# Optimization experiments

Hardware: AMD Instinct MI355X
Metric: run time of the kernel (lower is better)

## Reference

```python
import jax, jax.numpy as jnp
import numpy as np

H = 32  # hidden size per direction (hard-wired in module)


def _gru_scan(x_proj, W_hh, b_hh, reverse):
    """x_proj: [T, B, 3H] = x @ W_ih.T + b_ih (precomputed). Returns all hidden states [T, B, H].
    Gate order follows PyTorch: (r, z, n)."""
    def step(h, xp):
        gh = h @ W_hh.T + b_hh                      # [B, 3H]
        xr, xz, xn = jnp.split(xp, 3, axis=-1)
        hr, hz, hn = jnp.split(gh, 3, axis=-1)
        r = jax.nn.sigmoid(xr + hr)
        z = jax.nn.sigmoid(xz + hz)
        n = jnp.tanh(xn + r * hn)
        h_new = (1.0 - z) * n + z * h
        return h_new, h_new

    B = x_proj.shape[1]
    h0 = jnp.zeros((B, H), x_proj.dtype)
    _, ys = jax.lax.scan(step, h0, x_proj, reverse=reverse)
    return ys  # ys[t] = hidden after consuming x[t] (fwd) or x[T-1..t] (bwd)


def setup_inputs() -> dict:
    key = jax.random.key(0)
    ks = jax.random.split(key, 14)
    B, T = 2048, 512
    s_ih = 1.0 / np.sqrt(H)
    inp = {
        "x": jax.random.normal(ks[0], (B, T, 1), dtype=jnp.float32),
        # forward-direction GRU params (PyTorch layout: [3H, in], [3H, H], [3H])
        "W_ih_f": jax.random.uniform(ks[1], (3 * H, 1), jnp.float32, -s_ih, s_ih),
        "W_hh_f": jax.random.uniform(ks[2], (3 * H, H), jnp.float32, -s_ih, s_ih),
        "b_ih_f": jax.random.uniform(ks[3], (3 * H,), jnp.float32, -s_ih, s_ih),
        "b_hh_f": jax.random.uniform(ks[4], (3 * H,), jnp.float32, -s_ih, s_ih),
        # backward-direction GRU params
        "W_ih_b": jax.random.uniform(ks[5], (3 * H, 1), jnp.float32, -s_ih, s_ih),
        "W_hh_b": jax.random.uniform(ks[6], (3 * H, H), jnp.float32, -s_ih, s_ih),
        "b_ih_b": jax.random.uniform(ks[7], (3 * H,), jnp.float32, -s_ih, s_ih),
        "b_hh_b": jax.random.uniform(ks[8], (3 * H,), jnp.float32, -s_ih, s_ih),
        # MLP head: Linear(64,16) -> ReLU -> Linear(16,1) -> Sigmoid
        "W1": jax.random.uniform(ks[9], (16, 2 * H), jnp.float32, -0.125, 0.125),
        "b1": jax.random.uniform(ks[10], (16,), jnp.float32, -0.125, 0.125),
        "W2": jax.random.uniform(ks[11], (1, 16), jnp.float32, -0.25, 0.25),
        "b2": jax.random.uniform(ks[12], (1,), jnp.float32, -0.25, 0.25),
    }
    return inp


def reference(x, W_ih_f, W_hh_f, b_ih_f, b_hh_f,
              W_ih_b, W_hh_b, b_ih_b, b_hh_b,
              W1, b1, W2, b2):
    xt = jnp.swapaxes(x, 0, 1)                 # [T, B, 1]
    # Precompute input projections for all timesteps (input_size=1 so this is cheap)
    xpf = xt @ W_ih_f.T + b_ih_f               # [T, B, 3H]
    xpb = xt @ W_ih_b.T + b_ih_b               # [T, B, 3H]
    ys_f = _gru_scan(xpf, W_hh_f, b_hh_f, reverse=False)
    ys_b = _gru_scan(xpb, W_hh_b, b_hh_b, reverse=True)
    # out[:, -1, :] in torch = concat(fwd hidden at t=T-1, bwd hidden at t=T-1)
    out_last = jnp.concatenate([ys_f[-1], ys_b[-1]], axis=-1)   # [B, 64]
    h1 = jax.nn.relu(out_last @ W1.T + b1)                      # [B, 16]
    return jax.nn.sigmoid(h1 @ W2.T + b2)                       # [B, 1]
```

## Files before the change

### kernel.cpp

```cpp
#include <hip/hip_runtime.h>


typedef float vf2 __attribute__((ext_vector_type(2)));
typedef float vf4 __attribute__((ext_vector_type(4)));
typedef _Float16 f16;
typedef f16 h2 __attribute__((ext_vector_type(2)));
typedef f16 h8 __attribute__((ext_vector_type(8)));

#define TT 512
#define HH 32

#define PIN(v) asm volatile("" : "+v"(v))

#define LOG2E 1.44269504f

__device__ __forceinline__ float fast_sigm(float a) {
  return __builtin_amdgcn_rcpf(1.0f + __builtin_amdgcn_exp2f(-LOG2E * a));
}
__device__ __forceinline__ float fast_tanh(float a) {
  return __builtin_fmaf(-2.0f,
      __builtin_amdgcn_rcpf(1.0f + __builtin_amdgcn_exp2f(2.0f * LOG2E * a)),
      1.0f);
}

__device__ __forceinline__ h2 pack_h2(vf2 a, float s) {
  h2 r = {(f16)(a.x * s), (f16)(a.y * s)};
  return r;
}

#define LDW16(P, BASE, S) \
  h2 P##0=pack_h2(Wp[(BASE)+0],(S)),  P##1=pack_h2(Wp[(BASE)+1],(S)), \
     P##2=pack_h2(Wp[(BASE)+2],(S)),  P##3=pack_h2(Wp[(BASE)+3],(S)), \
     P##4=pack_h2(Wp[(BASE)+4],(S)),  P##5=pack_h2(Wp[(BASE)+5],(S)), \
     P##6=pack_h2(Wp[(BASE)+6],(S)),  P##7=pack_h2(Wp[(BASE)+7],(S)), \
     P##8=pack_h2(Wp[(BASE)+8],(S)),  P##9=pack_h2(Wp[(BASE)+9],(S)), \
     P##A=pack_h2(Wp[(BASE)+10],(S)), P##B=pack_h2(Wp[(BASE)+11],(S)), \
     P##C=pack_h2(Wp[(BASE)+12],(S)), P##D=pack_h2(Wp[(BASE)+13],(S)), \
     P##E=pack_h2(Wp[(BASE)+14],(S)), P##F=pack_h2(Wp[(BASE)+15],(S)); \
  PIN(P##0);PIN(P##1);PIN(P##2);PIN(P##3);PIN(P##4);PIN(P##5);PIN(P##6);PIN(P##7); \
  PIN(P##8);PIN(P##9);PIN(P##A);PIN(P##B);PIN(P##C);PIN(P##D);PIN(P##E);PIN(P##F)

#define FDOT16(A0, A1, P, SEED) \
  float A0 = __builtin_amdgcn_fdot2(q0, P##0, (SEED), false); \
  float A1 = __builtin_amdgcn_fdot2(q1, P##1, 0.0f, false); \
  A0 = __builtin_amdgcn_fdot2(q2, P##2, A0, false);  A1 = __builtin_amdgcn_fdot2(q3, P##3, A1, false); \
  A0 = __builtin_amdgcn_fdot2(q4, P##4, A0, false);  A1 = __builtin_amdgcn_fdot2(q5, P##5, A1, false); \
  A0 = __builtin_amdgcn_fdot2(q6, P##6, A0, false);  A1 = __builtin_amdgcn_fdot2(q7, P##7, A1, false); \
  A0 = __builtin_amdgcn_fdot2(q8, P##8, A0, false);  A1 = __builtin_amdgcn_fdot2(q9, P##9, A1, false); \
  A0 = __builtin_amdgcn_fdot2(qA, P##A, A0, false);  A1 = __builtin_amdgcn_fdot2(qB, P##B, A1, false); \
  A0 = __builtin_amdgcn_fdot2(qC, P##C, A0, false);  A1 = __builtin_amdgcn_fdot2(qD, P##D, A1, false); \
  A0 = __builtin_amdgcn_fdot2(qE, P##E, A0, false);  A1 = __builtin_amdgcn_fdot2(qF, P##F, A1, false)

__global__ __launch_bounds__(256)
__attribute__((amdgpu_waves_per_eu(1, 1)))
void gru_bidir_head(const float* __restrict__ X,
                    const float* __restrict__ Wih_f, const float* __restrict__ Whh_f,
                    const float* __restrict__ bih_f, const float* __restrict__ bhh_f,
                    const float* __restrict__ Wih_b,
                    const float* __restrict__ bih_b, const float* __restrict__ bhh_b,
                    const float* __restrict__ W1, const float* __restrict__ b1,
                    const float* __restrict__ W2, const float* __restrict__ b2,
                    float* __restrict__ out)
{
  __shared__ float xbuf[8][TT];
  __shared__ f16   hbuf[8][HH];
  __shared__ float obuf[8][64];

  const int g  = threadIdx.x & 31;
  const int rs = threadIdx.x >> 5;
  const int b  = (blockIdx.x << 3) + rs;

  const vf4* Xr4 = (const vf4*)(X + (size_t)b * TT);
  vf4* xb4 = (vf4*)&xbuf[rs][0];
  #pragma unroll
  for (int q = 0; q < 4; ++q) xb4[g + 32 * q] = Xr4[g + 32 * q];

  const vf2* Wp = (const vf2*)Whh_f;
  const float s1 = -LOG2E;
  const float s2 = 2.0f * LOG2E;
  LDW16(Wr, (g)        * 16, s1);
  LDW16(Wz, (HH + g)   * 16, s1);
  LDW16(Wn, (2*HH + g) * 16, s2);

  float xwr = Wih_f[g] * s1, xwz = Wih_f[HH + g] * s1, xwn = Wih_f[2*HH + g] * s2;
  float cbr = (bih_f[g]      + bhh_f[g])      * s1;
  float cbz = (bih_f[HH + g] + bhh_f[HH + g]) * s1;
  float cbn = bih_f[2*HH + g] * s2;
  float cbh = bhh_f[2*HH + g] * s2;
  PIN(xwr); PIN(xwz); PIN(xwn); PIN(cbr); PIN(cbz); PIN(cbn); PIN(cbh);

  float h = 0.0f;
  hbuf[rs][g] = (f16)0.0f;
  __builtin_amdgcn_wave_barrier();

  const h8*  hv = (const h8*)&hbuf[rs][0];
  const vf4* xv = (const vf4*)&xbuf[rs][0];
  vf4 x4 = xv[0];

  #pragma unroll 1
  for (int tg = 0; tg < TT / 4; ++tg) {
    const vf4 x4n = xv[tg + 1 < TT / 4 ? tg + 1 : tg];

    float sr0 = __builtin_fmaf(x4.x, xwr, cbr), sz0 = __builtin_fmaf(x4.x, xwz, cbz),
          sn0 = __builtin_fmaf(x4.x, xwn, cbn);
    float sr1 = __builtin_fmaf(x4.y, xwr, cbr), sz1 = __builtin_fmaf(x4.y, xwz, cbz),
          sn1 = __builtin_fmaf(x4.y, xwn, cbn);
    float sr2 = __builtin_fmaf(x4.z, xwr, cbr), sz2 = __builtin_fmaf(x4.z, xwz, cbz),
          sn2 = __builtin_fmaf(x4.z, xwn, cbn);
    float sr3 = __builtin_fmaf(x4.w, xwr, cbr), sz3 = __builtin_fmaf(x4.w, xwz, cbz),
          sn3 = __builtin_fmaf(x4.w, xwn, cbn);

    #pragma unroll
    for (int u = 0; u < 4; ++u) {
      const float sr = (u == 0) ? sr0 : (u == 1) ? sr1 : (u == 2) ? sr2 : sr3;
      const float sz = (u == 0) ? sz0 : (u == 1) ? sz1 : (u == 2) ? sz2 : sz3;
      const float sn = (u == 0) ? sn0 : (u == 1) ? sn1 : (u == 2) ? sn2 : sn3;

      const h8 H0 = hv[0], H1 = hv[1], H2 = hv[2], H3 = hv[3];
      const h2 q0 = {H0[0], H0[1]}, q1 = {H0[2], H0[3]}, q2 = {H0[4], H0[5]}, q3 = {H0[6], H0[7]},
               q4 = {H1[0], H1[1]}, q5 = {H1[2], H1[3]}, q6 = {H1[4], H1[5]}, q7 = {H1[6], H1[7]},
               q8 = {H2[0], H2[1]}, q9 = {H2[2], H2[3]}, qA = {H2[4], H2[5]}, qB = {H2[6], H2[7]},
               qC = {H3[0], H3[1]}, qD = {H3[2], H3[3]}, qE = {H3[4], H3[5]}, qF = {H3[6], H3[7]};

      FDOT16(Ra, Rb, Wr, sr);
      FDOT16(Za, Zb, Wz, sz);
      FDOT16(Na, Nb, Wn, cbh);

      const float ar = Ra + Rb;
      const float az = Za + Zb;
      const float r = __builtin_amdgcn_rcpf(1.0f + __builtin_amdgcn_exp2f(ar));
      const float z = __builtin_amdgcn_rcpf(1.0f + __builtin_amdgcn_exp2f(az));
      const float y = __builtin_fmaf(r, Na + Nb, sn);
      const float n = __builtin_fmaf(-2.0f,
          __builtin_amdgcn_rcpf(1.0f + __builtin_amdgcn_exp2f(y)), 1.0f);
      h = __builtin_fmaf(z, h - n, n);

      hbuf[rs][g] = (f16)h;
      __builtin_amdgcn_wave_barrier();
    }
    x4 = x4n;
  }

  const float xl  = xbuf[rs][TT - 1];
  const float rb  = fast_sigm(__builtin_fmaf(xl, Wih_b[g],      bih_b[g]      + bhh_b[g]));
  const float zb  = fast_sigm(__builtin_fmaf(xl, Wih_b[HH + g], bih_b[HH + g] + bhh_b[HH + g]));
  const float xnb = __builtin_fmaf(xl, Wih_b[2*HH + g], bih_b[2*HH + g]);
  const float nb  = fast_tanh(__builtin_fmaf(rb, bhh_b[2*HH + g], xnb));
  const float hb  = nb - zb * nb;

  obuf[rs][g]      = h;
  obuf[rs][32 + g] = hb;
  __builtin_amdgcn_wave_barrier();

  const int j = g & 15;
  const vf4* W1r = (const vf4*)(W1 + j * 64);
  const vf4* hc  = (const vf4*)&obuf[rs][0];
  vf4 a4 = W1r[0] * hc[0];
  #pragma unroll
  for (int q = 1; q < 16; ++q)
    a4 = __builtin_elementwise_fma(W1r[q], hc[q], a4);
  float acc = b1[j] + (a4.x + a4.y) + (a4.z + a4.w);
  float h1 = fmaxf(acc, 0.0f) * W2[j];
  h1 += __shfl_down(h1, 8, 16);
  h1 += __shfl_down(h1, 4, 16);
  h1 += __shfl_down(h1, 2, 16);
  h1 += __shfl_down(h1, 1, 16);
  if (g == 0) out[b] = fast_sigm(h1 + b2[0]);
}

extern "C" void kernel_launch(void* const* d_in, const int* in_sizes, int n_in,
                              void* d_out, int out_size, void* d_ws, size_t ws_size,
                              hipStream_t stream) {
  const float* X     = (const float*)d_in[0];
  const float* Wih_f = (const float*)d_in[1];
  const float* Whh_f = (const float*)d_in[2];
  const float* bih_f = (const float*)d_in[3];
  const float* bhh_f = (const float*)d_in[4];
  const float* Wih_b = (const float*)d_in[5];
  const float* bih_b = (const float*)d_in[7];
  const float* bhh_b = (const float*)d_in[8];
  const float* W1    = (const float*)d_in[9];
  const float* b1    = (const float*)d_in[10];
  const float* W2    = (const float*)d_in[11];
  const float* b2    = (const float*)d_in[12];
  float* out = (float*)d_out;

  gru_bidir_head<<<256, 256, 0, stream>>>(X, Wih_f, Whh_f, bih_f, bhh_f,
                                          Wih_b, bih_b, bhh_b, W1, b1, W2, b2, out);
}
```

Baseline: 174.7 us.

## Broadcast hidden state via DPP/swizzle lane exchange instead of LDS round-trip

Replaces the per-step LDS write/barrier/read of the fp16 hidden vector with an in-register all-gather built from DPP row operations and a ds_swizzle. Each lane receives the 32 hidden values in its own lane-dependent permuted order, so the weight packing is permuted to match. The aim is to cut LDS latency on the serial recurrence critical path. In exchange it adds about 16 DPP moves per step, one of which is a swizzle that still goes through the LDS unit, and it depends on the permutation being exactly right.

```diff
diff --git a/kernel.cpp b/kernel.cpp
--- a/kernel.cpp
+++ b/kernel.cpp
@@ -5,7 +5,6 @@
 typedef float vf4 __attribute__((ext_vector_type(4)));
 typedef _Float16 f16;
 typedef f16 h2 __attribute__((ext_vector_type(2)));
-typedef f16 h8 __attribute__((ext_vector_type(8)));
 
 #define TT 512
 #define HH 32
@@ -23,20 +22,32 @@
       1.0f);
 }
 
-__device__ __forceinline__ h2 pack_h2(vf2 a, float s) {
-  h2 r = {(f16)(a.x * s), (f16)(a.y * s)};
+template<int CTRL>
+__device__ __forceinline__ unsigned dppu(unsigned x) {
+  return (unsigned)__builtin_amdgcn_update_dpp((int)x, (int)x, CTRL, 0xF, 0xF, false);
+}
+__device__ __forceinline__ h2 bch2(unsigned x) {
+  union { unsigned u; h2 h; } c; c.u = x; return c.h;
+}
+
+__device__ __forceinline__ h2 packw(const vf2* Wp, int base, int pr, int oo,
+                                    int poff, int of, float s) {
+  vf2 e = Wp[base + (pr ^ poff)];
+  float lo = (oo ^ of) ? e.y : e.x;
+  float hi = (oo ^ of) ? e.x : e.y;
+  h2 r = {(f16)(lo * s), (f16)(hi * s)};
   return r;
 }
 
-#define LDW16(P, BASE, S) \
-  h2 P##0=pack_h2(Wp[(BASE)+0],(S)),  P##1=pack_h2(Wp[(BASE)+1],(S)), \
-     P##2=pack_h2(Wp[(BASE)+2],(S)),  P##3=pack_h2(Wp[(BASE)+3],(S)), \
-     P##4=pack_h2(Wp[(BASE)+4],(S)),  P##5=pack_h2(Wp[(BASE)+5],(S)), \
-     P##6=pack_h2(Wp[(BASE)+6],(S)),  P##7=pack_h2(Wp[(BASE)+7],(S)), \
-     P##8=pack_h2(Wp[(BASE)+8],(S)),  P##9=pack_h2(Wp[(BASE)+9],(S)), \
-     P##A=pack_h2(Wp[(BASE)+10],(S)), P##B=pack_h2(Wp[(BASE)+11],(S)), \
-     P##C=pack_h2(Wp[(BASE)+12],(S)), P##D=pack_h2(Wp[(BASE)+13],(S)), \
-     P##E=pack_h2(Wp[(BASE)+14],(S)), P##F=pack_h2(Wp[(BASE)+15],(S)); \
+#define LDWB(P, BASE, S) \
+  h2 P##0=packw(Wp,(BASE),pr,oo, 0,0,(S)), P##1=packw(Wp,(BASE),pr,oo, 1,0,(S)), \
+     P##2=packw(Wp,(BASE),pr,oo, 3,1,(S)), P##3=packw(Wp,(BASE),pr,oo, 2,1,(S)), \
+     P##4=packw(Wp,(BASE),pr,oo, 7,1,(S)), P##5=packw(Wp,(BASE),pr,oo, 6,1,(S)), \
+     P##6=packw(Wp,(BASE),pr,oo, 4,0,(S)), P##7=packw(Wp,(BASE),pr,oo, 5,0,(S)), \
+     P##8=packw(Wp,(BASE),pr,oo, 8,0,(S)), P##9=packw(Wp,(BASE),pr,oo, 9,0,(S)), \
+     P##A=packw(Wp,(BASE),pr,oo,11,1,(S)), P##B=packw(Wp,(BASE),pr,oo,10,1,(S)), \
+     P##C=packw(Wp,(BASE),pr,oo,15,1,(S)), P##D=packw(Wp,(BASE),pr,oo,14,1,(S)), \
+     P##E=packw(Wp,(BASE),pr,oo,12,0,(S)), P##F=packw(Wp,(BASE),pr,oo,13,0,(S)); \
   PIN(P##0);PIN(P##1);PIN(P##2);PIN(P##3);PIN(P##4);PIN(P##5);PIN(P##6);PIN(P##7); \
   PIN(P##8);PIN(P##9);PIN(P##A);PIN(P##B);PIN(P##C);PIN(P##D);PIN(P##E);PIN(P##F)
 
@@ -63,7 +74,6 @@
                     float* __restrict__ out)
 {
   __shared__ float xbuf[8][TT];
-  __shared__ f16   hbuf[8][HH];
   __shared__ float obuf[8][64];
 
   const int g  = threadIdx.x & 31;
@@ -78,9 +88,11 @@
   const vf2* Wp = (const vf2*)Whh_f;
   const float s1 = -LOG2E;
   const float s2 = 2.0f * LOG2E;
-  LDW16(Wr, (g)        * 16, s1);
-  LDW16(Wz, (HH + g)   * 16, s1);
-  LDW16(Wn, (2*HH + g) * 16, s2);
+  const int pr = g >> 1;
+  const int oo = g & 1;
+  LDWB(Wr, (g)        * 16, s1);
+  LDWB(Wz, (HH + g)   * 16, s1);
+  LDWB(Wn, (2*HH + g) * 16, s2);
 
   float xwr = Wih_f[g] * s1, xwz = Wih_f[HH + g] * s1, xwn = Wih_f[2*HH + g] * s2;
   float cbr = (bih_f[g]      + bhh_f[g])      * s1;
@@ -90,10 +102,7 @@
   PIN(xwr); PIN(xwz); PIN(xwn); PIN(cbr); PIN(cbz); PIN(cbn); PIN(cbh);
 
   float h = 0.0f;
-  hbuf[rs][g] = (f16)0.0f;
-  __builtin_amdgcn_wave_barrier();
-
-  const h8*  hv = (const h8*)&hbuf[rs][0];
+
   const vf4* xv = (const vf4*)&xbuf[rs][0];
   vf4 x4 = xv[0];
 
@@ -116,11 +125,29 @@
       const float sz = (u == 0) ? sz0 : (u == 1) ? sz1 : (u == 2) ? sz2 : sz3;
       const float sn = (u == 0) ? sn0 : (u == 1) ? sn1 : (u == 2) ? sn2 : sn3;
 
-      const h8 H0 = hv[0], H1 = hv[1], H2 = hv[2], H3 = hv[3];
-      const h2 q0 = {H0[0], H0[1]}, q1 = {H0[2], H0[3]}, q2 = {H0[4], H0[5]}, q3 = {H0[6], H0[7]},
-               q4 = {H1[0], H1[1]}, q5 = {H1[2], H1[3]}, q6 = {H1[4], H1[5]}, q7 = {H1[6], H1[7]},
-               q8 = {H2[0], H2[1]}, q9 = {H2[2], H2[3]}, qA = {H2[4], H2[5]}, qB = {H2[6], H2[7]},
-               qC = {H3[0], H3[1]}, qD = {H3[2], H3[3]}, qE = {H3[4], H3[5]}, qF = {H3[6], H3[7]};
+      unsigned uh; { union { f16 f; unsigned short u16; } cc; cc.f = (f16)h; uh = cc.u16; }
+      const unsigned T1 = dppu<0xB1>(uh);
+      const unsigned A0 = (uh & 0xffffu) | (T1 << 16);
+      const unsigned E0 = (unsigned)__builtin_amdgcn_ds_swizzle((int)A0, 0x401F);
+      const unsigned B0 = dppu<0x4E>(A0);
+      const unsigned C0 = dppu<0x141>(A0);
+      const unsigned C1 = dppu<0x141>(B0);
+      const unsigned D0 = dppu<0x140>(A0);
+      const unsigned D1 = dppu<0x140>(B0);
+      const unsigned D2 = dppu<0x140>(C0);
+      const unsigned D3 = dppu<0x140>(C1);
+      const unsigned F0 = dppu<0x4E>(E0);
+      const unsigned G0 = dppu<0x141>(E0);
+      const unsigned G1 = dppu<0x141>(F0);
+      const unsigned H0u = dppu<0x140>(E0);
+      const unsigned H1u = dppu<0x140>(F0);
+      const unsigned H2u = dppu<0x140>(G0);
+      const unsigned H3u = dppu<0x140>(G1);
+
+      const h2 q0 = bch2(A0),  q1 = bch2(B0),  q2 = bch2(C0),  q3 = bch2(C1),
+               q4 = bch2(D0),  q5 = bch2(D1),  q6 = bch2(D2),  q7 = bch2(D3),
+               q8 = bch2(E0),  q9 = bch2(F0),  qA = bch2(G0),  qB = bch2(G1),
+               qC = bch2(H0u), qD = bch2(H1u), qE = bch2(H2u), qF = bch2(H3u);
 
       FDOT16(Ra, Rb, Wr, sr);
       FDOT16(Za, Zb, Wz, sz);
@@ -134,9 +161,6 @@
       const float n = __builtin_fmaf(-2.0f,
           __builtin_amdgcn_rcpf(1.0f + __builtin_amdgcn_exp2f(y)), 1.0f);
       h = __builtin_fmaf(z, h - n, n);
-
-      hbuf[rs][g] = (f16)h;
-      __builtin_amdgcn_wave_barrier();
     }
     x4 = x4n;
   }
```

Result: slower. 188.7 us (+8.0%).

## Split GRU hidden dot products across wave halves with permlane32 swap reduction

Applied to the files above, without the earlier changes.

Each batch row now uses a full 64-lane wave instead of 32 lanes. Each half-wave computes the dot products over 16 of the 32 hidden inputs, and the partial sums are combined with v_permlane32_swap. The r and z sigmoids are split between the two halves and exchanged the same way. The aim is to halve the serial fdot2 chain on each recurrent step and run twice as many waves per CU (512-thread blocks). The cost is extra cross-lane swaps per step, a duplicated h store, and higher wave occupancy pressure on registers.

```diff
diff --git a/kernel.cpp b/kernel.cpp
--- a/kernel.cpp
+++ b/kernel.cpp
@@ -23,36 +23,36 @@
       1.0f);
 }
 
+#define SWAP2(LO, HI, X) \
+  float LO = (X), HI = (X); PIN(HI); \
+  asm volatile("v_permlane32_swap_b32 %0, %1" : "+v"(LO), "+v"(HI))
+
 __device__ __forceinline__ h2 pack_h2(vf2 a, float s) {
   h2 r = {(f16)(a.x * s), (f16)(a.y * s)};
   return r;
 }
 
-#define LDW16(P, BASE, S) \
-  h2 P##0=pack_h2(Wp[(BASE)+0],(S)),  P##1=pack_h2(Wp[(BASE)+1],(S)), \
-     P##2=pack_h2(Wp[(BASE)+2],(S)),  P##3=pack_h2(Wp[(BASE)+3],(S)), \
-     P##4=pack_h2(Wp[(BASE)+4],(S)),  P##5=pack_h2(Wp[(BASE)+5],(S)), \
-     P##6=pack_h2(Wp[(BASE)+6],(S)),  P##7=pack_h2(Wp[(BASE)+7],(S)), \
-     P##8=pack_h2(Wp[(BASE)+8],(S)),  P##9=pack_h2(Wp[(BASE)+9],(S)), \
-     P##A=pack_h2(Wp[(BASE)+10],(S)), P##B=pack_h2(Wp[(BASE)+11],(S)), \
-     P##C=pack_h2(Wp[(BASE)+12],(S)), P##D=pack_h2(Wp[(BASE)+13],(S)), \
-     P##E=pack_h2(Wp[(BASE)+14],(S)), P##F=pack_h2(Wp[(BASE)+15],(S)); \
-  PIN(P##0);PIN(P##1);PIN(P##2);PIN(P##3);PIN(P##4);PIN(P##5);PIN(P##6);PIN(P##7); \
-  PIN(P##8);PIN(P##9);PIN(P##A);PIN(P##B);PIN(P##C);PIN(P##D);PIN(P##E);PIN(P##F)
+#define LDW8(P, BASE, S) \
+  h2 P##0=pack_h2(Wp[(BASE)+kb+0],(S)), P##1=pack_h2(Wp[(BASE)+kb+1],(S)), \
+     P##2=pack_h2(Wp[(BASE)+kb+2],(S)), P##3=pack_h2(Wp[(BASE)+kb+3],(S)), \
+     P##4=pack_h2(Wp[(BASE)+kb+4],(S)), P##5=pack_h2(Wp[(BASE)+kb+5],(S)), \
+     P##6=pack_h2(Wp[(BASE)+kb+6],(S)), P##7=pack_h2(Wp[(BASE)+kb+7],(S)); \
+  PIN(P##0);PIN(P##1);PIN(P##2);PIN(P##3);PIN(P##4);PIN(P##5);PIN(P##6);PIN(P##7)
 
-#define FDOT16(A0, A1, P, SEED) \
-  float A0 = __builtin_amdgcn_fdot2(q0, P##0, (SEED), false); \
-  float A1 = __builtin_amdgcn_fdot2(q1, P##1, 0.0f, false); \
-  A0 = __builtin_amdgcn_fdot2(q2, P##2, A0, false);  A1 = __builtin_amdgcn_fdot2(q3, P##3, A1, false); \
-  A0 = __builtin_amdgcn_fdot2(q4, P##4, A0, false);  A1 = __builtin_amdgcn_fdot2(q5, P##5, A1, false); \
-  A0 = __builtin_amdgcn_fdot2(q6, P##6, A0, false);  A1 = __builtin_amdgcn_fdot2(q7, P##7, A1, false); \
-  A0 = __builtin_amdgcn_fdot2(q8, P##8, A0, false);  A1 = __builtin_amdgcn_fdot2(q9, P##9, A1, false); \
-  A0 = __builtin_amdgcn_fdot2(qA, P##A, A0, false);  A1 = __builtin_amdgcn_fdot2(qB, P##B, A1, false); \
-  A0 = __builtin_amdgcn_fdot2(qC, P##C, A0, false);  A1 = __builtin_amdgcn_fdot2(qD, P##D, A1, false); \
-  A0 = __builtin_amdgcn_fdot2(qE, P##E, A0, false);  A1 = __builtin_amdgcn_fdot2(qF, P##F, A1, false)
+#define FDOT8(OUT, P, SEED) \
+  float OUT; { \
+    float c0 = __builtin_amdgcn_fdot2(q0, P##0, (SEED), false); \
+    float c1 = __builtin_amdgcn_fdot2(q1, P##1, 0.0f, false); \
+    c0 = __builtin_amdgcn_fdot2(q2, P##2, c0, false); \
+    c1 = __builtin_amdgcn_fdot2(q3, P##3, c1, false); \
+    c0 = __builtin_amdgcn_fdot2(q4, P##4, c0, false); \
+    c1 = __builtin_amdgcn_fdot2(q5, P##5, c1, false); \
+    c0 = __builtin_amdgcn_fdot2(q6, P##6, c0, false); \
+    c1 = __builtin_amdgcn_fdot2(q7, P##7, c1, false); \
+    OUT = c0 + c1; }
 
-__global__ __launch_bounds__(256)
-__attribute__((amdgpu_waves_per_eu(1, 1)))
+__global__ __launch_bounds__(512)
+__attribute__((amdgpu_waves_per_eu(2)))
 void gru_bidir_head(const float* __restrict__ X,
                     const float* __restrict__ Wih_f, const float* __restrict__ Whh_f,
                     const float* __restrict__ bih_f, const float* __restrict__ bhh_f,
@@ -63,37 +63,41 @@
                     float* __restrict__ out)
 {
   __shared__ float xbuf[8][TT];
-  __shared__ f16   hbuf[8][HH];
+  __shared__ f16   hbuf[8][64];
   __shared__ float obuf[8][64];
 
-  const int g  = threadIdx.x & 31;
-  const int rs = threadIdx.x >> 5;
-  const int b  = (blockIdx.x << 3) + rs;
+  const int lane = threadIdx.x & 63;
+  const int g    = lane & 31;
+  const int hi   = lane >> 5;
+  const int kb   = 8 * hi;
+  const int rs   = threadIdx.x >> 6;
+  const int b    = (blockIdx.x << 3) + rs;
 
   const vf4* Xr4 = (const vf4*)(X + (size_t)b * TT);
   vf4* xb4 = (vf4*)&xbuf[rs][0];
   #pragma unroll
-  for (int q = 0; q < 4; ++q) xb4[g + 32 * q] = Xr4[g + 32 * q];
+  for (int q = 0; q < 2; ++q) xb4[lane + 64 * q] = Xr4[lane + 64 * q];
 
   const vf2* Wp = (const vf2*)Whh_f;
   const float s1 = -LOG2E;
   const float s2 = 2.0f * LOG2E;
-  LDW16(Wr, (g)        * 16, s1);
-  LDW16(Wz, (HH + g)   * 16, s1);
-  LDW16(Wn, (2*HH + g) * 16, s2);
+  LDW8(Wr, (g)        * 16, s1);
+  LDW8(Wz, (HH + g)   * 16, s1);
+  LDW8(Wn, (2*HH + g) * 16, s2);
 
-  float xwr = Wih_f[g] * s1, xwz = Wih_f[HH + g] * s1, xwn = Wih_f[2*HH + g] * s2;
-  float cbr = (bih_f[g]      + bhh_f[g])      * s1;
-  float cbz = (bih_f[HH + g] + bhh_f[HH + g]) * s1;
-  float cbn = bih_f[2*HH + g] * s2;
-  float cbh = bhh_f[2*HH + g] * s2;
-  PIN(xwr); PIN(xwz); PIN(xwn); PIN(cbr); PIN(cbz); PIN(cbn); PIN(cbh);
+  const float xwr_m = hi ? 0.0f : Wih_f[g] * s1;
+  const float cbr_m = hi ? 0.0f : (bih_f[g] + bhh_f[g]) * s1;
+  const float xwz_m = hi ? (Wih_f[HH + g] * s1) : 0.0f;
+  const float cbz_m = hi ? ((bih_f[HH + g] + bhh_f[HH + g]) * s1) : 0.0f;
+  const float cbh_m = hi ? 0.0f : bhh_f[2*HH + g] * s2;
+  const float xwn   = Wih_f[2*HH + g] * s2;
+  const float cbn   = bih_f[2*HH + g] * s2;
 
   float h = 0.0f;
-  hbuf[rs][g] = (f16)0.0f;
+  hbuf[rs][lane] = (f16)0.0f;
   __builtin_amdgcn_wave_barrier();
 
-  const h8*  hv = (const h8*)&hbuf[rs][0];
+  const h8* hv = (const h8*)(&hbuf[rs][0] + hi * 48);
   const vf4* xv = (const vf4*)&xbuf[rs][0];
   vf4 x4 = xv[0];
 
@@ -101,13 +105,13 @@
   for (int tg = 0; tg < TT / 4; ++tg) {
     const vf4 x4n = xv[tg + 1 < TT / 4 ? tg + 1 : tg];
 
-    float sr0 = __builtin_fmaf(x4.x, xwr, cbr), sz0 = __builtin_fmaf(x4.x, xwz, cbz),
+    float sr0 = __builtin_fmaf(x4.x, xwr_m, cbr_m), sz0 = __builtin_fmaf(x4.x, xwz_m, cbz_m),
           sn0 = __builtin_fmaf(x4.x, xwn, cbn);
-    float sr1 = __builtin_fmaf(x4.y, xwr, cbr), sz1 = __builtin_fmaf(x4.y, xwz, cbz),
+    float sr1 = __builtin_fmaf(x4.y, xwr_m, cbr_m), sz1 = __builtin_fmaf(x4.y, xwz_m, cbz_m),
           sn1 = __builtin_fmaf(x4.y, xwn, cbn);
-    float sr2 = __builtin_fmaf(x4.z, xwr, cbr), sz2 = __builtin_fmaf(x4.z, xwz, cbz),
+    float sr2 = __builtin_fmaf(x4.z, xwr_m, cbr_m), sz2 = __builtin_fmaf(x4.z, xwz_m, cbz_m),
           sn2 = __builtin_fmaf(x4.z, xwn, cbn);
-    float sr3 = __builtin_fmaf(x4.w, xwr, cbr), sz3 = __builtin_fmaf(x4.w, xwz, cbz),
+    float sr3 = __builtin_fmaf(x4.w, xwr_m, cbr_m), sz3 = __builtin_fmaf(x4.w, xwz_m, cbz_m),
           sn3 = __builtin_fmaf(x4.w, xwn, cbn);
 
     #pragma unroll
@@ -116,26 +120,30 @@
       const float sz = (u == 0) ? sz0 : (u == 1) ? sz1 : (u == 2) ? sz2 : sz3;
       const float sn = (u == 0) ? sn0 : (u == 1) ? sn1 : (u == 2) ? sn2 : sn3;
 
-      const h8 H0 = hv[0], H1 = hv[1], H2 = hv[2], H3 = hv[3];
-      const h2 q0 = {H0[0], H0[1]}, q1 = {H0[2], H0[3]}, q2 = {H0[4], H0[5]}, q3 = {H0[6], H0[7]},
-               q4 = {H1[0], H1[1]}, q5 = {H1[2], H1[3]}, q6 = {H1[4], H1[5]}, q7 = {H1[6], H1[7]},
-               q8 = {H2[0], H2[1]}, q9 = {H2[2], H2[3]}, qA = {H2[4], H2[5]}, qB = {H2[6], H2[7]},
-               qC = {H3[0], H3[1]}, qD = {H3[2], H3[3]}, qE = {H3[4], H3[5]}, qF = {H3[6], H3[7]};
+      const h8 H0 = hv[0], H1 = hv[1];
+      const h2 q0 = {H0[0], H0[1]}, q1 = {H0[2], H0[3]},
+               q2 = {H0[4], H0[5]}, q3 = {H0[6], H0[7]},
+               q4 = {H1[0], H1[1]}, q5 = {H1[2], H1[3]},
+               q6 = {H1[4], H1[5]}, q7 = {H1[6], H1[7]};
 
-      FDOT16(Ra, Rb, Wr, sr);
-      FDOT16(Za, Zb, Wz, sz);
-      FDOT16(Na, Nb, Wn, cbh);
+      FDOT8(Pr, Wr, sr);
+      FDOT8(Pz, Wz, sz);
+      FDOT8(Pn, Wn, cbh_m);
 
-      const float ar = Ra + Rb;
-      const float az = Za + Zb;
-      const float r = __builtin_amdgcn_rcpf(1.0f + __builtin_amdgcn_exp2f(ar));
-      const float z = __builtin_amdgcn_rcpf(1.0f + __builtin_amdgcn_exp2f(az));
-      const float y = __builtin_fmaf(r, Na + Nb, sn);
+      SWAP2(rlo, rhi, Pr);  const float ar = rlo + rhi;
+      SWAP2(zlo, zhi, Pz);  const float az = zlo + zhi;
+      SWAP2(nlo, nhi, Pn);  const float an = nlo + nhi;
+
+      const float sel = hi ? az : ar;
+      const float S = __builtin_amdgcn_rcpf(1.0f + __builtin_amdgcn_exp2f(sel));
+      SWAP2(rS, zS, S);
+
+      const float y = __builtin_fmaf(rS, an, sn);
       const float n = __builtin_fmaf(-2.0f,
           __builtin_amdgcn_rcpf(1.0f + __builtin_amdgcn_exp2f(y)), 1.0f);
-      h = __builtin_fmaf(z, h - n, n);
+      h = __builtin_fmaf(zS, h - n, n);
 
-      hbuf[rs][g] = (f16)h;
+      hbuf[rs][lane] = (f16)h;
       __builtin_amdgcn_wave_barrier();
     }
     x4 = x4n;
@@ -148,11 +156,10 @@
   const float nb  = fast_tanh(__builtin_fmaf(rb, bhh_b[2*HH + g], xnb));
   const float hb  = nb - zb * nb;
 
-  obuf[rs][g]      = h;
-  obuf[rs][32 + g] = hb;
+  obuf[rs][lane] = hi ? hb : h;
   __builtin_amdgcn_wave_barrier();
 
-  const int j = g & 15;
+  const int j = lane & 15;
   const vf4* W1r = (const vf4*)(W1 + j * 64);
   const vf4* hc  = (const vf4*)&obuf[rs][0];
   vf4 a4 = W1r[0] * hc[0];
@@ -165,7 +172,7 @@
   h1 += __shfl_down(h1, 4, 16);
   h1 += __shfl_down(h1, 2, 16);
   h1 += __shfl_down(h1, 1, 16);
-  if (g == 0) out[b] = fast_sigm(h1 + b2[0]);
+  if (lane == 0) out[b] = fast_sigm(h1 + b2[0]);
 }
 
 extern "C" void kernel_launch(void* const* d_in, const int* in_sizes, int n_in,
@@ -185,6 +192,6 @@
   const float* b2    = (const float*)d_in[12];
   float* out = (float*)d_out;
 
-  gru_bidir_head<<<256, 256, 0, stream>>>(X, Wih_f, Whh_f, bih_f, bhh_f,
+  gru_bidir_head<<<256, 512, 0, stream>>>(X, Wih_f, Whh_f, bih_f, bhh_f,
                                           Wih_b, bih_b, bhh_b, W1, b1, W2, b2, out);
 }
```

New measurement: 229.2 us. +31.2%, slower.

## Compute GRU recurrent matvec with MFMA over 16-sequence tiles

Applied to the files above, without the earlier changes.

Replaces the per-lane fdot2 recurrent matvec with 16x16x32 f16 MFMA instructions. Each 128-thread block now handles 16 batch rows, with two waves splitting the 96 gate rows. The hidden state is exchanged through double-buffered shared memory with a block-wide barrier every timestep. This cuts instruction count per step, but adds MFMA latency and __syncthreads on the serial critical path, and halves the grid to 128 blocks.

```diff
diff --git a/kernel.cpp b/kernel.cpp
--- a/kernel.cpp
+++ b/kernel.cpp
@@ -5,12 +5,14 @@
 typedef float vf4 __attribute__((ext_vector_type(4)));
 typedef _Float16 f16;
 typedef f16 h2 __attribute__((ext_vector_type(2)));
+typedef f16 h4 __attribute__((ext_vector_type(4)));
 typedef f16 h8 __attribute__((ext_vector_type(8)));
 
 #define TT 512
 #define HH 32
-
-#define PIN(v) asm volatile("" : "+v"(v))
+#define XPAD 516
+#define HXPAD 36
+#define OPAD 68
 
 #define LOG2E 1.44269504f
 
@@ -22,36 +24,18 @@
       __builtin_amdgcn_rcpf(1.0f + __builtin_amdgcn_exp2f(2.0f * LOG2E * a)),
       1.0f);
 }
-
 __device__ __forceinline__ h2 pack_h2(vf2 a, float s) {
   h2 r = {(f16)(a.x * s), (f16)(a.y * s)};
   return r;
 }
 
-#define LDW16(P, BASE, S) \
-  h2 P##0=pack_h2(Wp[(BASE)+0],(S)),  P##1=pack_h2(Wp[(BASE)+1],(S)), \
-     P##2=pack_h2(Wp[(BASE)+2],(S)),  P##3=pack_h2(Wp[(BASE)+3],(S)), \
-     P##4=pack_h2(Wp[(BASE)+4],(S)),  P##5=pack_h2(Wp[(BASE)+5],(S)), \
-     P##6=pack_h2(Wp[(BASE)+6],(S)),  P##7=pack_h2(Wp[(BASE)+7],(S)), \
-     P##8=pack_h2(Wp[(BASE)+8],(S)),  P##9=pack_h2(Wp[(BASE)+9],(S)), \
-     P##A=pack_h2(Wp[(BASE)+10],(S)), P##B=pack_h2(Wp[(BASE)+11],(S)), \
-     P##C=pack_h2(Wp[(BASE)+12],(S)), P##D=pack_h2(Wp[(BASE)+13],(S)), \
-     P##E=pack_h2(Wp[(BASE)+14],(S)), P##F=pack_h2(Wp[(BASE)+15],(S)); \
-  PIN(P##0);PIN(P##1);PIN(P##2);PIN(P##3);PIN(P##4);PIN(P##5);PIN(P##6);PIN(P##7); \
-  PIN(P##8);PIN(P##9);PIN(P##A);PIN(P##B);PIN(P##C);PIN(P##D);PIN(P##E);PIN(P##F)
+#define LDA(P, ROW, S) \
+  h8 P; { const vf2* rp = Wp + (size_t)(ROW) * 16; \
+    const h2 a0 = pack_h2(rp[2*q],     (S)), a1 = pack_h2(rp[2*q+1],   (S)); \
+    const h2 a2 = pack_h2(rp[8+2*q],   (S)), a3 = pack_h2(rp[8+2*q+1], (S)); \
+    P = (h8){a0.x, a0.y, a1.x, a1.y, a2.x, a2.y, a3.x, a3.y}; }
 
-#define FDOT16(A0, A1, P, SEED) \
-  float A0 = __builtin_amdgcn_fdot2(q0, P##0, (SEED), false); \
-  float A1 = __builtin_amdgcn_fdot2(q1, P##1, 0.0f, false); \
-  A0 = __builtin_amdgcn_fdot2(q2, P##2, A0, false);  A1 = __builtin_amdgcn_fdot2(q3, P##3, A1, false); \
-  A0 = __builtin_amdgcn_fdot2(q4, P##4, A0, false);  A1 = __builtin_amdgcn_fdot2(q5, P##5, A1, false); \
-  A0 = __builtin_amdgcn_fdot2(q6, P##6, A0, false);  A1 = __builtin_amdgcn_fdot2(q7, P##7, A1, false); \
-  A0 = __builtin_amdgcn_fdot2(q8, P##8, A0, false);  A1 = __builtin_amdgcn_fdot2(q9, P##9, A1, false); \
-  A0 = __builtin_amdgcn_fdot2(qA, P##A, A0, false);  A1 = __builtin_amdgcn_fdot2(qB, P##B, A1, false); \
-  A0 = __builtin_amdgcn_fdot2(qC, P##C, A0, false);  A1 = __builtin_amdgcn_fdot2(qD, P##D, A1, false); \
-  A0 = __builtin_amdgcn_fdot2(qE, P##E, A0, false);  A1 = __builtin_amdgcn_fdot2(qF, P##F, A1, false)
-
-__global__ __launch_bounds__(256)
+__global__ __launch_bounds__(128)
 __attribute__((amdgpu_waves_per_eu(1, 1)))
 void gru_bidir_head(const float* __restrict__ X,
                     const float* __restrict__ Wih_f, const float* __restrict__ Whh_f,
@@ -62,110 +46,121 @@
                     const float* __restrict__ W2, const float* __restrict__ b2,
                     float* __restrict__ out)
 {
-  __shared__ float xbuf[8][TT];
-  __shared__ f16   hbuf[8][HH];
-  __shared__ float obuf[8][64];
+  __shared__ float xbuf[16][XPAD];
+  __shared__ f16   hx[2][16][HXPAD];
+  __shared__ float obuf[16][OPAD];
 
-  const int g  = threadIdx.x & 31;
-  const int rs = threadIdx.x >> 5;
-  const int b  = (blockIdx.x << 3) + rs;
+  const int tid  = threadIdx.x;
+  const int lane = tid & 63;
+  const int Wv   = tid >> 6;
+  const int bq   = lane & 15;
+  const int q    = lane >> 4;
+  const int rb   = blockIdx.x << 4;
 
-  const vf4* Xr4 = (const vf4*)(X + (size_t)b * TT);
-  vf4* xb4 = (vf4*)&xbuf[rs][0];
-  #pragma unroll
-  for (int q = 0; q < 4; ++q) xb4[g + 32 * q] = Xr4[g + 32 * q];
+  #pragma unroll 4
+  for (int r = 0; r < 16; ++r)
+    ((vf4*)&xbuf[r][0])[tid] = ((const vf4*)(X + (size_t)(rb + r) * TT))[tid];
 
   const vf2* Wp = (const vf2*)Whh_f;
   const float s1 = -LOG2E;
   const float s2 = 2.0f * LOG2E;
-  LDW16(Wr, (g)        * 16, s1);
-  LDW16(Wz, (HH + g)   * 16, s1);
-  LDW16(Wn, (2*HH + g) * 16, s2);
+  const int mrow = 16*Wv + bq;
+  LDA(Ar, mrow,      s1);
+  LDA(Az, 32 + mrow, s1);
+  LDA(An, 64 + mrow, s2);
 
-  float xwr = Wih_f[g] * s1, xwz = Wih_f[HH + g] * s1, xwn = Wih_f[2*HH + g] * s2;
-  float cbr = (bih_f[g]      + bhh_f[g])      * s1;
-  float cbz = (bih_f[HH + g] + bhh_f[HH + g]) * s1;
-  float cbn = bih_f[2*HH + g] * s2;
-  float cbh = bhh_f[2*HH + g] * s2;
-  PIN(xwr); PIN(xwz); PIN(xwn); PIN(cbr); PIN(cbz); PIN(cbn); PIN(cbh);
+  const int j0 = 16*Wv + 4*q;
+  vf4 xwr, cbr4, xwz, cbz4, xwn4, cbn4, Cn;
+  #pragma unroll
+  for (int r = 0; r < 4; ++r) {
+    const int j = j0 + r;
+    xwr[r]  = Wih_f[j] * s1;
+    cbr4[r] = (bih_f[j] + bhh_f[j]) * s1;
+    xwz[r]  = Wih_f[HH + j] * s1;
+    cbz4[r] = (bih_f[HH + j] + bhh_f[HH + j]) * s1;
+    xwn4[r] = Wih_f[2*HH + j] * s2;
+    cbn4[r] = bih_f[2*HH + j] * s2;
+    Cn[r]   = bhh_f[2*HH + j] * s2;
+  }
 
-  float h = 0.0f;
-  hbuf[rs][g] = (f16)0.0f;
-  __builtin_amdgcn_wave_barrier();
+  __syncthreads();
 
-  const h8*  hv = (const h8*)&hbuf[rs][0];
-  const vf4* xv = (const vf4*)&xbuf[rs][0];
-  vf4 x4 = xv[0];
+  vf4 hold = {0.0f, 0.0f, 0.0f, 0.0f};
+  h8  B = {};
+  const vf4* xrow = (const vf4*)&xbuf[bq][0];
+  vf4 x4 = xrow[0];
 
   #pragma unroll 1
   for (int tg = 0; tg < TT / 4; ++tg) {
-    const vf4 x4n = xv[tg + 1 < TT / 4 ? tg + 1 : tg];
-
-    float sr0 = __builtin_fmaf(x4.x, xwr, cbr), sz0 = __builtin_fmaf(x4.x, xwz, cbz),
-          sn0 = __builtin_fmaf(x4.x, xwn, cbn);
-    float sr1 = __builtin_fmaf(x4.y, xwr, cbr), sz1 = __builtin_fmaf(x4.y, xwz, cbz),
-          sn1 = __builtin_fmaf(x4.y, xwn, cbn);
-    float sr2 = __builtin_fmaf(x4.z, xwr, cbr), sz2 = __builtin_fmaf(x4.z, xwz, cbz),
-          sn2 = __builtin_fmaf(x4.z, xwn, cbn);
-    float sr3 = __builtin_fmaf(x4.w, xwr, cbr), sz3 = __builtin_fmaf(x4.w, xwz, cbz),
-          sn3 = __builtin_fmaf(x4.w, xwn, cbn);
+    const vf4 x4n = xrow[tg + 1 < TT / 4 ? tg + 1 : tg];
 
     #pragma unroll
     for (int u = 0; u < 4; ++u) {
-      const float sr = (u == 0) ? sr0 : (u == 1) ? sr1 : (u == 2) ? sr2 : sr3;
-      const float sz = (u == 0) ? sz0 : (u == 1) ? sz1 : (u == 2) ? sz2 : sz3;
-      const float sn = (u == 0) ? sn0 : (u == 1) ? sn1 : (u == 2) ? sn2 : sn3;
+      const float xb = (u == 0) ? x4.x : (u == 1) ? x4.y : (u == 2) ? x4.z : x4.w;
 
-      const h8 H0 = hv[0], H1 = hv[1], H2 = hv[2], H3 = hv[3];
-      const h2 q0 = {H0[0], H0[1]}, q1 = {H0[2], H0[3]}, q2 = {H0[4], H0[5]}, q3 = {H0[6], H0[7]},
-               q4 = {H1[0], H1[1]}, q5 = {H1[2], H1[3]}, q6 = {H1[4], H1[5]}, q7 = {H1[6], H1[7]},
-               q8 = {H2[0], H2[1]}, q9 = {H2[2], H2[3]}, qA = {H2[4], H2[5]}, qB = {H2[6], H2[7]},
-               qC = {H3[0], H3[1]}, qD = {H3[2], H3[3]}, qE = {H3[4], H3[5]}, qF = {H3[6], H3[7]};
+      const vf4 Cr = { __builtin_fmaf(xb, xwr.x, cbr4.x), __builtin_fmaf(xb, xwr.y, cbr4.y),
+                       __builtin_fmaf(xb, xwr.z, cbr4.z), __builtin_fmaf(xb, xwr.w, cbr4.w) };
+      const vf4 Cz = { __builtin_fmaf(xb, xwz.x, cbz4.x), __builtin_fmaf(xb, xwz.y, cbz4.y),
+                       __builtin_fmaf(xb, xwz.z, cbz4.z), __builtin_fmaf(xb, xwz.w, cbz4.w) };
+      const vf4 sn = { __builtin_fmaf(xb, xwn4.x, cbn4.x), __builtin_fmaf(xb, xwn4.y, cbn4.y),
+                       __builtin_fmaf(xb, xwn4.z, cbn4.z), __builtin_fmaf(xb, xwn4.w, cbn4.w) };
 
-      FDOT16(Ra, Rb, Wr, sr);
-      FDOT16(Za, Zb, Wz, sz);
-      FDOT16(Na, Nb, Wn, cbh);
+      const vf4 Dr = __builtin_amdgcn_mfma_f32_16x16x32_f16(Ar, B, Cr, 0, 0, 0);
+      const vf4 Dz = __builtin_amdgcn_mfma_f32_16x16x32_f16(Az, B, Cz, 0, 0, 0);
+      const vf4 Dn = __builtin_amdgcn_mfma_f32_16x16x32_f16(An, B, Cn, 0, 0, 0);
 
-      const float ar = Ra + Rb;
-      const float az = Za + Zb;
-      const float r = __builtin_amdgcn_rcpf(1.0f + __builtin_amdgcn_exp2f(ar));
-      const float z = __builtin_amdgcn_rcpf(1.0f + __builtin_amdgcn_exp2f(az));
-      const float y = __builtin_fmaf(r, Na + Nb, sn);
-      const float n = __builtin_fmaf(-2.0f,
-          __builtin_amdgcn_rcpf(1.0f + __builtin_amdgcn_exp2f(y)), 1.0f);
-      h = __builtin_fmaf(z, h - n, n);
+      #pragma unroll
+      for (int r = 0; r < 4; ++r) {
+        const float rr = __builtin_amdgcn_rcpf(1.0f + __builtin_amdgcn_exp2f(Dr[r]));
+        const float zz = __builtin_amdgcn_rcpf(1.0f + __builtin_amdgcn_exp2f(Dz[r]));
+        const float y  = __builtin_fmaf(rr, Dn[r], sn[r]);
+        const float nn = __builtin_fmaf(-2.0f,
+            __builtin_amdgcn_rcpf(1.0f + __builtin_amdgcn_exp2f(y)), 1.0f);
+        hold[r] = __builtin_fmaf(zz, hold[r] - nn, nn);
+      }
 
-      hbuf[rs][g] = (f16)h;
-      __builtin_amdgcn_wave_barrier();
+      const h4 own = { (f16)hold.x, (f16)hold.y, (f16)hold.z, (f16)hold.w };
+      *(h4*)&hx[u & 1][bq][16*Wv + 4*q] = own;
+      __syncthreads();
+      const h4 lo = *(const h4*)&hx[u & 1][bq][4*q];
+      const h4 hi = *(const h4*)&hx[u & 1][bq][16 + 4*q];
+      B = (h8){lo[0], lo[1], lo[2], lo[3], hi[0], hi[1], hi[2], hi[3]};
     }
     x4 = x4n;
   }
 
-  const float xl  = xbuf[rs][TT - 1];
-  const float rb  = fast_sigm(__builtin_fmaf(xl, Wih_b[g],      bih_b[g]      + bhh_b[g]));
-  const float zb  = fast_sigm(__builtin_fmaf(xl, Wih_b[HH + g], bih_b[HH + g] + bhh_b[HH + g]));
-  const float xnb = __builtin_fmaf(xl, Wih_b[2*HH + g], bih_b[2*HH + g]);
-  const float nb  = fast_tanh(__builtin_fmaf(rb, bhh_b[2*HH + g], xnb));
-  const float hb  = nb - zb * nb;
+  *(vf4*)&obuf[bq][16*Wv + 4*q] = hold;
+  __syncthreads();
 
-  obuf[rs][g]      = h;
-  obuf[rs][32 + g] = hb;
-  __builtin_amdgcn_wave_barrier();
+  const int g   = tid & 31;
+  const int grp = tid >> 5;
+  #pragma unroll 1
+  for (int it = 0; it < 4; ++it) {
+    const int row = grp + 4 * it;
+    const float xl  = xbuf[row][TT - 1];
+    const float rbv = fast_sigm(__builtin_fmaf(xl, Wih_b[g],      bih_b[g]      + bhh_b[g]));
+    const float zbv = fast_sigm(__builtin_fmaf(xl, Wih_b[HH + g], bih_b[HH + g] + bhh_b[HH + g]));
+    const float xnb = __builtin_fmaf(xl, Wih_b[2*HH + g], bih_b[2*HH + g]);
+    const float nbv = fast_tanh(__builtin_fmaf(rbv, bhh_b[2*HH + g], xnb));
+    const float hbv = nbv - zbv * nbv;
+    obuf[row][32 + g] = hbv;
+    __builtin_amdgcn_wave_barrier();
 
-  const int j = g & 15;
-  const vf4* W1r = (const vf4*)(W1 + j * 64);
-  const vf4* hc  = (const vf4*)&obuf[rs][0];
-  vf4 a4 = W1r[0] * hc[0];
-  #pragma unroll
-  for (int q = 1; q < 16; ++q)
-    a4 = __builtin_elementwise_fma(W1r[q], hc[q], a4);
-  float acc = b1[j] + (a4.x + a4.y) + (a4.z + a4.w);
-  float h1 = fmaxf(acc, 0.0f) * W2[j];
-  h1 += __shfl_down(h1, 8, 16);
-  h1 += __shfl_down(h1, 4, 16);
-  h1 += __shfl_down(h1, 2, 16);
-  h1 += __shfl_down(h1, 1, 16);
-  if (g == 0) out[b] = fast_sigm(h1 + b2[0]);
+    const int jj = g & 15;
+    const vf4* W1r = (const vf4*)(W1 + jj * 64);
+    const vf4* hc  = (const vf4*)&obuf[row][0];
+    vf4 a4 = W1r[0] * hc[0];
+    #pragma unroll
+    for (int qq = 1; qq < 16; ++qq)
+      a4 = __builtin_elementwise_fma(W1r[qq], hc[qq], a4);
+    float acc = b1[jj] + (a4.x + a4.y) + (a4.z + a4.w);
+    float h1v = fmaxf(acc, 0.0f) * W2[jj];
+    h1v += __shfl_down(h1v, 8, 16);
+    h1v += __shfl_down(h1v, 4, 16);
+    h1v += __shfl_down(h1v, 2, 16);
+    h1v += __shfl_down(h1v, 1, 16);
+    if (g == 0) out[rb + row] = fast_sigm(h1v + b2[0]);
+  }
 }
 
 extern "C" void kernel_launch(void* const* d_in, const int* in_sizes, int n_in,
@@ -185,6 +180,6 @@
   const float* b2    = (const float*)d_in[12];
   float* out = (float*)d_out;
 
-  gru_bidir_head<<<256, 256, 0, stream>>>(X, Wih_f, Whh_f, bih_f, bhh_f,
+  gru_bidir_head<<<128, 128, 0, stream>>>(X, Wih_f, Whh_f, bih_f, bhh_f,
                                           Wih_b, bih_b, bhh_b, W1, b1, W2, b2, out);
 }
```

Result: slower. 219.8 us (+25.8%).
